# Kernel tuning notes

Measured on AMD Instinct MI355X. Metric: run time of the kernel, lower is better.

## Reference

```python
import jax, jax.numpy as jnp
import numpy as np

V, N, T, H, DK, DV, FF = 32000, 512, 43, 1024, 512, 512, 4096
EPS = 1e-5

def setup_inputs() -> dict:
    key = jax.random.key(0)
    ks = jax.random.split(key, 16)
    s = 0.02
    def p(k, shape):
        return jax.random.normal(k, shape, jnp.float32) * s
    return {
        "inputs": jax.random.randint(ks[0], (N, T), 0, V),
        "emb": p(ks[1], (V, H)),
        "pos": p(ks[2], (T, H)),
        "q1_w": p(ks[3], (H, DK)), "q1_b": jnp.zeros((DK,), jnp.float32),
        "k1_w": p(ks[4], (H, DK)), "k1_b": jnp.zeros((DK,), jnp.float32),
        "v1_w": p(ks[5], (H, DV)), "v1_b": jnp.zeros((DV,), jnp.float32),
        "q2_w": p(ks[6], (H, DK)), "q2_b": jnp.zeros((DK,), jnp.float32),
        "k2_w": p(ks[7], (H, DK)), "k2_b": jnp.zeros((DK,), jnp.float32),
        "v2_w": p(ks[8], (H, DV)), "v2_b": jnp.zeros((DV,), jnp.float32),
        "proj_w": p(ks[9], (2 * DV, H)), "proj_b": jnp.zeros((H,), jnp.float32),
        "ln_g": jnp.ones((H,), jnp.float32), "ln_b": jnp.zeros((H,), jnp.float32),
        "w1_w": p(ks[10], (H, FF)), "w1_b": jnp.zeros((FF,), jnp.float32),
        "w2_w": p(ks[11], (FF, H)), "w2_b": jnp.zeros((H,), jnp.float32),
        "fl_w": p(ks[12], (H, 1)), "fl_b": jnp.zeros((1,), jnp.float32),
    }

def reference(inputs, emb, pos, q1_w, q1_b, k1_w, k1_b, v1_w, v1_b,
              q2_w, q2_b, k2_w, k2_b, v2_w, v2_b, proj_w, proj_b,
              ln_g, ln_b, w1_w, w1_b, w2_w, w2_b, fl_w, fl_b):
    # embed: token + positional embeddings -> (N, T, H)
    x = emb[inputs] + pos[None, :, :]

    def ln(y):
        m = y.mean(-1, keepdims=True)
        v = ((y - m) ** 2).mean(-1, keepdims=True)  # unbiased=False, as torch LayerNorm
        return (y - m) / jnp.sqrt(v + EPS) * ln_g + ln_b

    def head(qw, qb, kw, kb, vw, vb):
        Q = x @ qw + qb            # (N,T,DK)
        K = x @ kw + kb            # (N,T,DK)
        Vh = x @ vw + vb           # (N,T,DV)
        scores = jnp.einsum('ntd,nsd->nts', Q, K) / jnp.sqrt(jnp.float32(DK))
        return jnp.einsum('nts,nsd->ntd', jax.nn.softmax(scores, axis=-1), Vh)

    attn = jnp.concatenate(
        [head(q1_w, q1_b, k1_w, k1_b, v1_w, v1_b),
         head(q2_w, q2_b, k2_w, k2_b, v2_w, v2_b)], axis=-1)  # (N,T,2*DV)
    h = ln(x + attn @ proj_w + proj_b)
    # FFN with ReLU (clamp(min=0)); NOTE: same LayerNorm params (norm_mh) reused
    h = ln(h + jnp.maximum(h @ w1_w + w1_b, 0.0) @ w2_w + w2_b)
    # final: sigmoid head on CLS (first) token -> (N,1)
    return jax.nn.sigmoid(h[:, 0, :] @ fl_w + fl_b)
```

## Files before the change

kernel.cpp:

```cpp
#include <hip/hip_runtime.h>
#include <math.h>

typedef float  f32x4  __attribute__((ext_vector_type(4)));
typedef short  bf16x8 __attribute__((ext_vector_type(8)));
typedef unsigned short u16;
typedef unsigned int   u32;
typedef unsigned short u16x2 __attribute__((ext_vector_type(2)));
typedef unsigned short u16x4 __attribute__((ext_vector_type(4)));
typedef unsigned short u16x8 __attribute__((ext_vector_type(8)));

constexpr int Tn = 43, Hd = 1024, Nb = 512;

__device__ __forceinline__ u16 f2bf(float f) {
    u32 u = __float_as_uint(f);
    u32 r = u + 0x7FFFu + ((u >> 16) & 1u);
    return (u16)(r >> 16);
}
__device__ __forceinline__ float bf2f(u16 h) {
    return __uint_as_float(((u32)h) << 16);
}
__device__ __forceinline__ void cvt8(const float* f, u16x8* hi, u16x8* lo) {
    #pragma unroll
    for (int j = 0; j < 8; ++j) {
        u16 h = f2bf(f[j]);
        (*hi)[j] = h;
        (*lo)[j] = f2bf(f[j] - bf2f(h));
    }
}
__device__ __forceinline__ void cvt8h(const float* f, u16x8* hi) {
    #pragma unroll
    for (int j = 0; j < 8; ++j) (*hi)[j] = f2bf(f[j]);
}

__device__ __forceinline__ void convT1_seg(const float* __restrict__ W,
                                           u16* __restrict__ Hi,
                                           int K, int N, int local, int t, char* lds)
{
    float (*tile)[33] = (float(*)[33])lds;
    const int tn = N >> 5;
    const int k0 = (local / tn) << 5, n0 = (local % tn) << 5;
    {
        int kk = t >> 3, nn = (t & 7) * 4;
        float4 v = *(const float4*)(W + (size_t)(k0 + kk) * N + n0 + nn);
        tile[kk][nn] = v.x; tile[kk][nn + 1] = v.y;
        tile[kk][nn + 2] = v.z; tile[kk][nn + 3] = v.w;
    }
    __syncthreads();
    {
        int nn = t >> 3, kk = (t & 7) * 4;
        u16x4 h;
        #pragma unroll
        for (int j = 0; j < 4; ++j) h[j] = f2bf(tile[kk + j][nn]);
        *(u16x4*)(Hi + (size_t)(n0 + nn) * K + k0 + kk) = h;
    }
}

__device__ __forceinline__ void convN1_seg(const float* __restrict__ src,
                                           u16* __restrict__ Hi, int local, int t)
{
    const size_t e = ((size_t)local * 256 + t) * 8;
    const float4* p = (const float4*)(src + e);
    float4 v0 = p[0], v1 = p[1];
    float f[8] = {v0.x, v0.y, v0.z, v0.w, v1.x, v1.y, v1.z, v1.w};
    u16x8 hv;
    cvt8h(f, &hv);
    *(u16x8*)(Hi + e) = hv;
}

__device__ __forceinline__ void gemm_dev(
    const u16* Ahi, const u16* Alo, int lda, size_t az,
    const u16* Bhi, int ldb, size_t bz,
    const float* bias, float* C, u16* CHi, u16* CLo, int ldc, int crz, int ccz,
    int M, int N, int K, int nz, int flags,
    float* Cp, size_t pstride, char* lds, int tid, int t0, int tstride)
{
    const bool RELU = flags & 1, PLANES = flags & 2, SPLIT = flags & 4;
    const bool A1 = flags & 8, PL1 = flags & 16;
    const int ncol = N >> 7;
    const int tpz = (M >> 6) * ncol;
    const int ntiles = nz * tpz;
    const int BOFF = A1 ? 8192 : 16384;

    const int ra = tid >> 2, ga = tid & 3;
    const int rb = tid >> 1, gb = (tid & 1) << 1;
    const int wA  = ((ra >> 4) << 10) | (ga << 8) | ((((ra & 15) ^ (ga << 1)) & 15) << 4);
    const int wB0 = ((rb >> 4) << 10) | (gb << 8) | ((((rb & 15) ^ (gb << 1)) & 15) << 4);
    const int wB1 = ((rb >> 4) << 10) | ((gb + 1) << 8) | ((((rb & 15) ^ ((gb + 1) << 1)) & 15) << 4);
    const int wv = tid >> 6, lane = tid & 63;
    const int wr = wv >> 1, wc = wv & 1;
    const int l15 = lane & 15, l4 = lane >> 4;
    const int rsw = (l15 ^ (l4 << 1)) << 4;
    int fA[2], fB[4];
    #pragma unroll
    for (int m = 0; m < 2; ++m) fA[m] = (((wr << 1) + m) << 10) | (l4 << 8) | rsw;
    #pragma unroll
    for (int n = 0; n < 4; ++n) fB[n] = (((wc << 2) + n) << 10) | (l4 << 8) | rsw;

    for (int t = t0; t < ntiles; t += tstride) {
        const int z = t / tpz, r = t - z * tpz;
        const int tm = r / ncol;
        const int bm = tm << 6, bn = (r - tm * ncol) << 7;
        int kc = K, kb = 0;
        const u16 *ah = Ahi, *al = Alo, *bh = Bhi;
        if (SPLIT) { kc = K / nz; kb = z * kc; }
        else { ah += z * az; if (!A1) al += z * az; bh += z * bz; }

        const u16* pAh = ah + (size_t)(bm + ra) * lda + kb + ga * 8;
        const u16* pAl = A1 ? pAh : al + (size_t)(bm + ra) * lda + kb + ga * 8;
        const u16* pBh = bh + (size_t)(bn + rb) * ldb + kb + gb * 8;

        f32x4 acc[2][4] = {};

        uint4 sAh0 = *(const uint4*)pAh,        sAh1 = *(const uint4*)(pAh + 32);
        uint4 sAl0, sAl1;
        if (!A1) { sAl0 = *(const uint4*)pAl;   sAl1 = *(const uint4*)(pAl + 32); }
        uint4 sB00 = *(const uint4*)pBh,        sB01 = *(const uint4*)(pBh + 8);
        uint4 sB10 = *(const uint4*)(pBh + 32), sB11 = *(const uint4*)(pBh + 40);

        for (int k0 = 0; k0 < kc; k0 += 64) {
            __syncthreads();
            *(uint4*)(lds + wA)        = sAh0;
            *(uint4*)(lds + 4096 + wA) = sAh1;
            if (!A1) {
                *(uint4*)(lds + 8192 + wA)  = sAl0;
                *(uint4*)(lds + 12288 + wA) = sAl1;
            }
            *(uint4*)(lds + BOFF + wB0)        = sB00;
            *(uint4*)(lds + BOFF + wB1)        = sB01;
            *(uint4*)(lds + BOFF + 8192 + wB0) = sB10;
            *(uint4*)(lds + BOFF + 8192 + wB1) = sB11;
            __syncthreads();
            if (k0 + 64 < kc) {
                pAh += 64; pBh += 64;
                sAh0 = *(const uint4*)pAh;        sAh1 = *(const uint4*)(pAh + 32);
                if (!A1) {
                    pAl += 64;
                    sAl0 = *(const uint4*)pAl;    sAl1 = *(const uint4*)(pAl + 32);
                }
                sB00 = *(const uint4*)pBh;        sB01 = *(const uint4*)(pBh + 8);
                sB10 = *(const uint4*)(pBh + 32); sB11 = *(const uint4*)(pBh + 40);
            }
            #pragma unroll
            for (int h = 0; h < 2; ++h) {
                bf16x8 a8[2], c8[2], b8[4];
                #pragma unroll
                for (int m = 0; m < 2; ++m) {
                    a8[m] = *(const bf16x8*)(lds + (h << 12) + fA[m]);
                    if (!A1) c8[m] = *(const bf16x8*)(lds + 8192 + (h << 12) + fA[m]);
                }
                #pragma unroll
                for (int n = 0; n < 4; ++n)
                    b8[n] = *(const bf16x8*)(lds + BOFF + (h << 13) + fB[n]);
                #pragma unroll
                for (int m = 0; m < 2; ++m)
                    #pragma unroll
                    for (int n = 0; n < 4; ++n) {
                        acc[m][n] = __builtin_amdgcn_mfma_f32_16x16x32_bf16(a8[m], b8[n], acc[m][n], 0, 0, 0);
                        if (!A1)
                            acc[m][n] = __builtin_amdgcn_mfma_f32_16x16x32_bf16(c8[m], b8[n], acc[m][n], 0, 0, 0);
                    }
            }
        }

        #pragma unroll
        for (int n = 0; n < 4; ++n) {
            const int col = bn + (wc << 6) + n * 16 + l15;
            const float bv = (!SPLIT && bias) ? bias[col] : 0.f;
            const int colz = SPLIT ? col : col + z * ccz;
            #pragma unroll
            for (int m = 0; m < 2; ++m) {
                const int row0 = bm + (wr << 5) + m * 16 + l4 * 4;
                #pragma unroll
                for (int rg = 0; rg < 4; ++rg) {
                    const int row = row0 + rg;
                    float v = acc[m][n][rg];
                    if (SPLIT) {
                        Cp[z * pstride + (size_t)row * N + col] = v;
                    } else {
                        const int rowz = row + z * crz;
                        v += bv;
                        if (RELU) v = fmaxf(v, 0.f);
                        if (PL1) {
                            CHi[(size_t)rowz * ldc + colz] = f2bf(v);
                        } else if (PLANES) {
                            u16 hh = f2bf(v);
                            CHi[(size_t)rowz * ldc + colz] = hh;
                            CLo[(size_t)rowz * ldc + colz] = f2bf(v - bf2f(hh));
                        } else {
                            C[(size_t)rowz * ldc + colz] = v;
                        }
                    }
                }
            }
        }
    }
}

__device__ __forceinline__ void gemm_G(
    const float* k1w, const float* k2w, const float* q1w, const float* q2w,
    u16* GHi, char* lds, int tid, int t0, int tstride)
{
    const int ra = tid >> 2, ga = tid & 3;
    const int rb = tid >> 1, gb = (tid & 1) << 1;
    const int wA  = ((ra >> 4) << 10) | (ga << 8) | ((((ra & 15) ^ (ga << 1)) & 15) << 4);
    const int wB0 = ((rb >> 4) << 10) | (gb << 8) | ((((rb & 15) ^ (gb << 1)) & 15) << 4);
    const int wB1 = ((rb >> 4) << 10) | ((gb + 1) << 8) | ((((rb & 15) ^ ((gb + 1) << 1)) & 15) << 4);
    const int wv = tid >> 6, lane = tid & 63;
    const int wr = wv >> 1, wc = wv & 1;
    const int l15 = lane & 15, l4 = lane >> 4;
    const int rsw = (l15 ^ (l4 << 1)) << 4;
    int fA[2], fB[4];
    #pragma unroll
    for (int m = 0; m < 2; ++m) fA[m] = (((wr << 1) + m) << 10) | (l4 << 8) | rsw;
    #pragma unroll
    for (int n = 0; n < 4; ++n) fB[n] = (((wc << 2) + n) << 10) | (l4 << 8) | rsw;

    for (int t = t0; t < 256; t += tstride) {
        const int z = t >> 7, r = t & 127;
        const int bm = (r >> 3) << 6, bn = (r & 7) << 7;
        const float* pA = (z ? k2w : k1w) + (size_t)(bm + ra) * 512 + ga * 8;
        const float* pB = (z ? q2w : q1w) + (size_t)(bn + rb) * 512 + gb * 8;

        f32x4 acc[2][4] = {};
        float4 a0 = ((const float4*)pA)[0], a1 = ((const float4*)pA)[1];
        float4 b0 = ((const float4*)pB)[0], b1 = ((const float4*)pB)[1];
        float4 b2 = ((const float4*)pB)[2], b3 = ((const float4*)pB)[3];

        for (int k0 = 0; k0 < 512; k0 += 32) {
            u16x8 hi, lo;
            float fa[8] = {a0.x, a0.y, a0.z, a0.w, a1.x, a1.y, a1.z, a1.w};
            float fb[8] = {b0.x, b0.y, b0.z, b0.w, b1.x, b1.y, b1.z, b1.w};
            float fc[8] = {b2.x, b2.y, b2.z, b2.w, b3.x, b3.y, b3.z, b3.w};
            __syncthreads();
            cvt8(fa, &hi, &lo);
            *(u16x8*)(lds + wA) = hi;
            *(u16x8*)(lds + 4096 + wA) = lo;
            cvt8h(fb, &hi);
            *(u16x8*)(lds + 8192 + wB0) = hi;
            cvt8h(fc, &hi);
            *(u16x8*)(lds + 8192 + wB1) = hi;
            __syncthreads();
            if (k0 + 32 < 512) {
                pA += 32; pB += 32;
                a0 = ((const float4*)pA)[0]; a1 = ((const float4*)pA)[1];
                b0 = ((const float4*)pB)[0]; b1 = ((const float4*)pB)[1];
                b2 = ((const float4*)pB)[2]; b3 = ((const float4*)pB)[3];
            }
            bf16x8 a8[2], c8[2], b8[4];
            #pragma unroll
            for (int m = 0; m < 2; ++m) {
                a8[m] = *(const bf16x8*)(lds + fA[m]);
                c8[m] = *(const bf16x8*)(lds + 4096 + fA[m]);
            }
            #pragma unroll
            for (int n = 0; n < 4; ++n)
                b8[n] = *(const bf16x8*)(lds + 8192 + fB[n]);
            #pragma unroll
            for (int m = 0; m < 2; ++m)
                #pragma unroll
                for (int n = 0; n < 4; ++n) {
                    acc[m][n] = __builtin_amdgcn_mfma_f32_16x16x32_bf16(a8[m], b8[n], acc[m][n], 0, 0, 0);
                    acc[m][n] = __builtin_amdgcn_mfma_f32_16x16x32_bf16(c8[m], b8[n], acc[m][n], 0, 0, 0);
                }
        }

        #pragma unroll
        for (int n = 0; n < 4; ++n) {
            const int col = bn + (wc << 6) + n * 16 + l15;
            #pragma unroll
            for (int m = 0; m < 2; ++m) {
                const int row0 = bm + (wr << 5) + m * 16 + l4 * 4;
                #pragma unroll
                for (int rg = 0; rg < 4; ++rg) {
                    const int row = z * 1024 + row0 + rg;
                    GHi[(size_t)row * 1024 + col] = f2bf(acc[m][n][rg]);
                }
            }
        }
    }
}

struct Args {
    const int* toks; const float* emb; const float* pos;
    const float *q1w, *q2w, *k1w, *k2w, *v1w, *v2w, *pw, *w1w, *w2w;
    const float *q1b, *q2b, *v1b, *v2b, *pb, *lg, *lb, *w1b, *w2b, *flw, *flb;
    u16 *GHi, *WpTHi, *W1THi, *W2THi, *WvNHi, *WvpHi;
    float *bU, *bvp;
    float* XclsF; u16 *XclsHi, *XclsLo;
    float* U; u16 *YHi, *YLo;
    float* Hb; u16 *HbHi, *HbLo;
    u16 *EHi, *ELo;
    float* Cp;
    float* out;
};

__global__ __launch_bounds__(256, 4)
void k1_kernel(Args A)
{
    __shared__ alignas(16) char lds[16384];
    const int id = blockIdx.x, t = threadIdx.x;
    const size_t HO = (size_t)1024 * 512;
    if (id < 256) {
        gemm_G(A.k1w, A.k2w, A.q1w, A.q2w, A.GHi, lds, t, id, 256);
    } else if (id < 768) {
        const int n = id - 256;
        const int tok = A.toks[n * Tn];
        float4 e = ((const float4*)(A.emb + (size_t)tok * Hd))[t];
        float4 p = ((const float4*)A.pos)[t];
        float f[4] = {e.x + p.x, e.y + p.y, e.z + p.z, e.w + p.w};
        ((float4*)(A.XclsF + (size_t)n * Hd))[t] = make_float4(f[0], f[1], f[2], f[3]);
        u16x4 hv, lv;
        #pragma unroll
        for (int j = 0; j < 4; ++j) {
            u16 h = f2bf(f[j]);
            hv[j] = h;
            lv[j] = f2bf(f[j] - bf2f(h));
        }
        *(u16x4*)(A.XclsHi + (size_t)n * Hd + t * 4) = hv;
        *(u16x4*)(A.XclsLo + (size_t)n * Hd + t * 4) = lv;
    } else if (id < 1280) {
        const int b = id - 768;
        const int wave = t >> 6, lane = t & 63;
        const int jj = b * 4 + wave;
        const int head = jj >> 10, j = jj & 1023;
        const float* row = (head ? A.k2w : A.k1w) + (size_t)j * 512;
        const float* bqp = head ? A.q2b : A.q1b;
        float4 r0 = ((const float4*)row)[lane * 2];
        float4 r1 = ((const float4*)row)[lane * 2 + 1];
        float4 b0 = ((const float4*)bqp)[lane * 2];
        float4 b1 = ((const float4*)bqp)[lane * 2 + 1];
        float d = r0.x*b0.x + r0.y*b0.y + r0.z*b0.z + r0.w*b0.w
                + r1.x*b1.x + r1.y*b1.y + r1.z*b1.z + r1.w*b1.w;
        #pragma unroll
        for (int off = 32; off; off >>= 1) d += __shfl_xor(d, off);
        if (lane == 0) A.bU[jj] = d;
    } else if (id < 2304) {
        convT1_seg(A.pw, A.WpTHi, 1024, 1024, id - 1280, t, lds);
    } else if (id < 2560) {
        convN1_seg(A.v1w, A.WvNHi, id - 2304, t);
    } else {
        convN1_seg(A.v2w, A.WvNHi + HO, id - 2560, t);
    }
}

__global__ __launch_bounds__(256, 4)
void k2_kernel(Args A)
{
    __shared__ alignas(16) char lds[32768];
    const int id = blockIdx.x, t = threadIdx.x;
    const size_t HO = (size_t)1024 * 512;
    if (id < 128)
        gemm_dev(A.XclsHi, A.XclsLo, 1024, 0, A.GHi, 1024, 0,
                 A.bU, A.U, nullptr, nullptr, 2048, 0, 0,
                 512, 2048, 1024, 1, 0, nullptr, 0, lds, t, id, 128);
    else if (id < 384)
        gemm_dev(A.WpTHi, nullptr, 1024, 512, A.WvNHi, 512, HO,
                 nullptr, nullptr, A.WvpHi, nullptr, 2048, 0, 1024,
                 1024, 1024, 512, 2, 8 | 16, nullptr, 0, lds, t, id - 128, 256);
    else if (id < 640) {
        const int wave = t >> 6, lane = t & 63;
        const int c = (id - 384) * 4 + wave;
        const int j0 = lane * 16;
        u16x8 h0 = *(const u16x8*)(A.WpTHi + (size_t)c * 1024 + j0);
        u16x8 h1 = *(const u16x8*)(A.WpTHi + (size_t)c * 1024 + j0 + 8);
        const float* bsrc = (j0 < 512) ? (A.v1b + j0) : (A.v2b + j0 - 512);
        float d = 0.f;
        #pragma unroll
        for (int j = 0; j < 8; ++j) d += bsrc[j] * bf2f(h0[j]);
        #pragma unroll
        for (int j = 0; j < 8; ++j) d += bsrc[8 + j] * bf2f(h1[j]);
        #pragma unroll
        for (int off = 32; off; off >>= 1) d += __shfl_xor(d, off);
        if (lane == 0) A.bvp[c] = d + A.pb[c];
    } else {
        convT1_seg(A.w1w, A.W1THi, 1024, 4096, id - 640, t, lds);
    }
}

__global__ __launch_bounds__(512, 1)
void k3_kernel(Args A)
{
    __shared__ float us[2048];
    __shared__ float ps[128];
    __shared__ u16 xc[Tn * 1024];
    const int n = blockIdx.x, tid = threadIdx.x;
    ((float4*)us)[tid] = ((const float4*)(A.U + (size_t)n * 2048))[tid];
    __syncthreads();

    const int wave = tid >> 6, lane = tid & 63;
    const int* tk = A.toks + n * Tn;
    for (int s = wave; s < Tn; s += 8) {
        const int tok = tk[s];
        const float4* er = (const float4*)(A.emb + (size_t)tok * Hd);
        const float4* pr = (const float4*)(A.pos + (size_t)s * Hd);
        float d1 = 0.f, d2 = 0.f;
        #pragma unroll
        for (int i = 0; i < 4; ++i) {
            const int c = i * 64 + lane;
            float4 e = er[c], p = pr[c];
            float x0 = e.x + p.x, x1 = e.y + p.y, x2 = e.z + p.z, x3 = e.w + p.w;
            u16x4 xv;
            xv[0] = f2bf(x0); xv[1] = f2bf(x1); xv[2] = f2bf(x2); xv[3] = f2bf(x3);
            *(u16x4*)(xc + s * 1024 + c * 4) = xv;
            const float* u1 = us + c * 4;
            const float* u2 = us + 1024 + c * 4;
            d1 += x0 * u1[0] + x1 * u1[1] + x2 * u1[2] + x3 * u1[3];
            d2 += x0 * u2[0] + x1 * u2[1] + x2 * u2[2] + x3 * u2[3];
        }
        #pragma unroll
        for (int off = 32; off; off >>= 1) {
            d1 += __shfl_xor(d1, off);
            d2 += __shfl_xor(d2, off);
        }
        if (lane == 0) {
            ps[s]      = d1 * 0.044194173824159216f;
            ps[64 + s] = d2 * 0.044194173824159216f;
        }
    }
    __syncthreads();
    if (wave < 2) {
        float v = (lane < Tn) ? ps[wave * 64 + lane] : -INFINITY;
        float mx = v;
        #pragma unroll
        for (int off = 32; off; off >>= 1) mx = fmaxf(mx, __shfl_xor(mx, off));
        float e = (lane < Tn) ? __expf(v - mx) : 0.f;
        float sum = e;
        #pragma unroll
        for (int off = 32; off; off >>= 1) sum += __shfl_xor(sum, off);
        if (lane < Tn) ps[wave * 64 + lane] = e / sum;
    }
    __syncthreads();

    float a1x = 0.f, a1y = 0.f, a2x = 0.f, a2y = 0.f;
    for (int s = 0; s < Tn; ++s) {
        const float p1 = ps[s], p2 = ps[64 + s];
        u16x2 xv = *(const u16x2*)(xc + s * 1024 + tid * 2);
        const float x0 = bf2f(xv[0]), x1 = bf2f(xv[1]);
        a1x = fmaf(p1, x0, a1x); a1y = fmaf(p1, x1, a1y);
        a2x = fmaf(p2, x0, a2x); a2y = fmaf(p2, x1, a2y);
    }
    u16x2 h1, l1, h2, l2;
    u16 h;
    h = f2bf(a1x); h1[0] = h; l1[0] = f2bf(a1x - bf2f(h));
    h = f2bf(a1y); h1[1] = h; l1[1] = f2bf(a1y - bf2f(h));
    h = f2bf(a2x); h2[0] = h; l2[0] = f2bf(a2x - bf2f(h));
    h = f2bf(a2y); h2[1] = h; l2[1] = f2bf(a2y - bf2f(h));
    const size_t o = (size_t)n * 2048 + tid * 2;
    *(u16x2*)(A.YHi + o) = h1;          *(u16x2*)(A.YLo + o) = l1;
    *(u16x2*)(A.YHi + o + 1024) = h2;   *(u16x2*)(A.YLo + o + 1024) = l2;
}

__global__ __launch_bounds__(256, 4)
void k4_kernel(Args A)
{
    __shared__ alignas(16) char lds[32768];
    const int id = blockIdx.x, t = threadIdx.x;
    if (id < 512)
        gemm_dev(A.YHi, A.YLo, 2048, 0, A.WvpHi, 2048, 0,
                 nullptr, nullptr, nullptr, nullptr, 0, 0, 0,
                 512, 1024, 2048, 8, 4, A.Cp, (size_t)Nb * Hd, lds, t, id, 512);
    else
        convT1_seg(A.w2w, A.W2THi, 4096, 1024, id - 512, t, lds);
}

__global__ __launch_bounds__(256)
void k5_kernel(Args A)
{
    const int tid = threadIdx.x;
    const size_t base = (size_t)blockIdx.x * Hd;
    const size_t P = (size_t)Nb * Hd;
    float4 v = ((const float4*)A.bvp)[tid];
    {
        float4 xc = ((const float4*)(A.XclsF + base))[tid];
        v.x += xc.x; v.y += xc.y; v.z += xc.z; v.w += xc.w;
    }
    #pragma unroll
    for (int z = 0; z < 8; ++z) {
        float4 c = ((const float4*)(A.Cp + z * P + base))[tid];
        v.x += c.x; v.y += c.y; v.z += c.z; v.w += c.w;
    }
    float s = v.x + v.y + v.z + v.w;
    float q = v.x*v.x + v.y*v.y + v.z*v.z + v.w*v.w;
    #pragma unroll
    for (int off = 32; off; off >>= 1) {
        s += __shfl_xor(s, off);
        q += __shfl_xor(q, off);
    }
    __shared__ float ss[4], sq[4];
    const int lane = tid & 63, w = tid >> 6;
    if (lane == 0) { ss[w] = s; sq[w] = q; }
    __syncthreads();
    s = ss[0] + ss[1] + ss[2] + ss[3];
    q = sq[0] + sq[1] + sq[2] + sq[3];
    const float mean = s * (1.f / Hd);
    const float var = q * (1.f / Hd) - mean * mean;
    const float rstd = rsqrtf(var + 1e-5f);
    float4 gv = ((const float4*)A.lg)[tid];
    float4 bv = ((const float4*)A.lb)[tid];
    float f[4];
    f[0] = (v.x - mean) * rstd * gv.x + bv.x;
    f[1] = (v.y - mean) * rstd * gv.y + bv.y;
    f[2] = (v.z - mean) * rstd * gv.z + bv.z;
    f[3] = (v.w - mean) * rstd * gv.w + bv.w;
    ((float4*)(A.Hb + base))[tid] = make_float4(f[0], f[1], f[2], f[3]);
    u16x4 hv, lv;
    #pragma unroll
    for (int j = 0; j < 4; ++j) {
        u16 hh = f2bf(f[j]);
        hv[j] = hh;
        lv[j] = f2bf(f[j] - bf2f(hh));
    }
    *(u16x4*)(A.HbHi + base + tid * 4) = hv;
    *(u16x4*)(A.HbLo + base + tid * 4) = lv;
}

__global__ __launch_bounds__(256, 4)
void k6_kernel(Args A)
{
    __shared__ alignas(16) char lds[32768];
    gemm_dev(A.HbHi, A.HbLo, 1024, 0, A.W1THi, 1024, 0,
             A.w1b, nullptr, A.EHi, A.ELo, 4096, 0, 0,
             512, 4096, 1024, 1, 3, nullptr, 0, lds, threadIdx.x, blockIdx.x, 256);
}

__global__ __launch_bounds__(256, 4)
void k7_kernel(Args A)
{
    __shared__ alignas(16) char lds[32768];
    gemm_dev(A.EHi, A.ELo, 4096, 0, A.W2THi, 4096, 0,
             nullptr, nullptr, nullptr, nullptr, 0, 0, 0,
             512, 1024, 4096, 4, 4, A.Cp, (size_t)Nb * Hd,
             lds, threadIdx.x, blockIdx.x, 256);
}

__global__ __launch_bounds__(256)
void k8_kernel(Args A)
{
    const int tid = threadIdx.x;
    const size_t base = (size_t)blockIdx.x * Hd;
    const size_t P = (size_t)Nb * Hd;
    float4 v = ((const float4*)A.w2b)[tid];
    {
        float4 hh = ((const float4*)(A.Hb + base))[tid];
        v.x += hh.x; v.y += hh.y; v.z += hh.z; v.w += hh.w;
    }
    #pragma unroll
    for (int z = 0; z < 4; ++z) {
        float4 c = ((const float4*)(A.Cp + z * P + base))[tid];
        v.x += c.x; v.y += c.y; v.z += c.z; v.w += c.w;
    }
    float s = v.x + v.y + v.z + v.w;
    float q = v.x*v.x + v.y*v.y + v.z*v.z + v.w*v.w;
    #pragma unroll
    for (int off = 32; off; off >>= 1) {
        s += __shfl_xor(s, off);
        q += __shfl_xor(q, off);
    }
    __shared__ float ss[4], sq[4], sd[4];
    const int lane = tid & 63, w = tid >> 6;
    if (lane == 0) { ss[w] = s; sq[w] = q; }
    __syncthreads();
    s = ss[0] + ss[1] + ss[2] + ss[3];
    q = sq[0] + sq[1] + sq[2] + sq[3];
    const float mean = s * (1.f / Hd);
    const float var = q * (1.f / Hd) - mean * mean;
    const float rstd = rsqrtf(var + 1e-5f);
    float4 gv = ((const float4*)A.lg)[tid];
    float4 bv = ((const float4*)A.lb)[tid];
    float4 wv = ((const float4*)A.flw)[tid];
    float d = ((v.x - mean) * rstd * gv.x + bv.x) * wv.x
            + ((v.y - mean) * rstd * gv.y + bv.y) * wv.y
            + ((v.z - mean) * rstd * gv.z + bv.z) * wv.z
            + ((v.w - mean) * rstd * gv.w + bv.w) * wv.w;
    #pragma unroll
    for (int off = 32; off; off >>= 1) d += __shfl_xor(d, off);
    if (lane == 0) sd[w] = d;
    __syncthreads();
    if (tid == 0) {
        float z = sd[0] + sd[1] + sd[2] + sd[3] + A.flb[0];
        A.out[blockIdx.x] = 1.f / (1.f + expf(-z));
    }
}

extern "C" void kernel_launch(void* const* d_in, const int* in_sizes, int n_in,
                              void* d_out, int out_size, void* d_ws, size_t ws_size,
                              hipStream_t stream)
{
    Args A;
    A.toks = (const int*)d_in[0];
    A.emb  = (const float*)d_in[1];
    A.pos  = (const float*)d_in[2];
    A.q1w = (const float*)d_in[3];  A.q1b = (const float*)d_in[4];
    A.k1w = (const float*)d_in[5];
    A.v1w = (const float*)d_in[7];  A.v1b = (const float*)d_in[8];
    A.q2w = (const float*)d_in[9];  A.q2b = (const float*)d_in[10];
    A.k2w = (const float*)d_in[11];
    A.v2w = (const float*)d_in[13]; A.v2b = (const float*)d_in[14];
    A.pw  = (const float*)d_in[15]; A.pb  = (const float*)d_in[16];
    A.lg  = (const float*)d_in[17]; A.lb  = (const float*)d_in[18];
    A.w1w = (const float*)d_in[19]; A.w1b = (const float*)d_in[20];
    A.w2w = (const float*)d_in[21]; A.w2b = (const float*)d_in[22];
    A.flw = (const float*)d_in[23]; A.flb = (const float*)d_in[24];
    A.out = (float*)d_out;
    char* wsb = (char*)d_ws;

    size_t off = 0;
    auto alloc = [&](size_t bytes) { size_t o = off; off = (off + bytes + 255) & ~(size_t)255; return o; };

    A.GHi   = (u16*)(wsb + alloc(2048 * 1024 * 2));
    A.WpTHi = (u16*)(wsb + alloc(1024 * 1024 * 2));
    A.W1THi = (u16*)(wsb + alloc(4096 * 1024 * 2));
    A.W2THi = (u16*)(wsb + alloc(1024 * 4096 * 2));
    A.WvNHi = (u16*)(wsb + alloc(2 * 1024 * 512 * 2));
    A.WvpHi = (u16*)(wsb + alloc(1024 * 2048 * 2));
    A.bU    = (float*)(wsb + alloc(2048 * 4));
    A.bvp   = (float*)(wsb + alloc(1024 * 4));
    A.XclsF = (float*)(wsb + alloc((size_t)Nb * Hd * 4));
    A.XclsHi= (u16*)(wsb + alloc((size_t)Nb * Hd * 2));
    A.XclsLo= (u16*)(wsb + alloc((size_t)Nb * Hd * 2));
    A.U     = (float*)(wsb + alloc((size_t)Nb * 2048 * 4));
    A.YHi   = (u16*)(wsb + alloc((size_t)Nb * 2048 * 2));
    A.YLo   = (u16*)(wsb + alloc((size_t)Nb * 2048 * 2));
    A.Hb    = (float*)(wsb + alloc((size_t)Nb * Hd * 4));
    A.HbHi  = (u16*)(wsb + alloc((size_t)Nb * Hd * 2));
    A.HbLo  = (u16*)(wsb + alloc((size_t)Nb * Hd * 2));
    A.EHi   = (u16*)(wsb + alloc((size_t)Nb * 4096 * 2));
    A.ELo   = (u16*)(wsb + alloc((size_t)Nb * 4096 * 2));
    A.Cp    = (float*)(wsb + alloc((size_t)8 * Nb * Hd * 4));

    k1_kernel<<<2816, 256, 0, stream>>>(A);
    k2_kernel<<<4736, 256, 0, stream>>>(A);
    k3_kernel<<<512,  512, 0, stream>>>(A);
    k4_kernel<<<4608, 256, 0, stream>>>(A);
    k5_kernel<<<512,  256, 0, stream>>>(A);
    k6_kernel<<<256,  256, 0, stream>>>(A);
    k7_kernel<<<256,  256, 0, stream>>>(A);
    k8_kernel<<<512,  256, 0, stream>>>(A);
}
```

Before: 114.4 us.

## Fuse residual+LayerNorm epilogues into split-K GEMMs via last-block atomic counters

Removes the separate k5 and k8 LayerNorm kernels. Each split-K GEMM block now increments a per-row-tile atomic counter, and the last block to finish a 64-row tile reduces the partials, applies LayerNorm and, in the final stage, the sigmoid head. This saves two kernel launches and their scheduling gaps. The cost is a serialized tail in which one block handles 64 rows on its own, plus a memset of the counters and reliance on the ordering that threadfence provides.

```diff
diff --git a/kernel.cpp b/kernel.cpp
--- a/kernel.cpp
+++ b/kernel.cpp
@@ -287,10 +287,12 @@
     u16 *GHi, *WpTHi, *W1THi, *W2THi, *WvNHi, *WvpHi;
     float *bU, *bvp;
     float* XclsF; u16 *XclsHi, *XclsLo;
-    float* U; u16 *YHi, *YLo;
+    u16 *YHi, *YLo;
+    float* U;
     float* Hb; u16 *HbHi, *HbLo;
     u16 *EHi, *ELo;
     float* Cp;
+    int *cnt1, *cnt2;
     float* out;
 };
 
@@ -455,63 +457,67 @@
 {
     __shared__ alignas(16) char lds[32768];
     const int id = blockIdx.x, t = threadIdx.x;
-    if (id < 512)
+    const size_t P = (size_t)Nb * Hd;
+    if (id < 512) {
         gemm_dev(A.YHi, A.YLo, 2048, 0, A.WvpHi, 2048, 0,
                  nullptr, nullptr, nullptr, nullptr, 0, 0, 0,
-                 512, 1024, 2048, 8, 4, A.Cp, (size_t)Nb * Hd, lds, t, id, 512);
-    else
+                 512, 1024, 2048, 8, 4, A.Cp, P, lds, t, id, 512);
+        const int tm = (id & 63) >> 3;
+        __threadfence();
+        int* flag = (int*)lds;
+        if (t == 0) *flag = atomicAdd(A.cnt1 + tm, 1);
+        __syncthreads();
+        if (*flag == 63) {
+            __threadfence();
+            float* shr = (float*)(lds + 64);
+            const int lane = t & 63, w = t >> 6;
+            for (int row = tm * 64; row < tm * 64 + 64; ++row) {
+                const size_t base = (size_t)row * Hd;
+                float4 v = ((const float4*)A.bvp)[t];
+                float4 xcv = ((const float4*)(A.XclsF + base))[t];
+                v.x += xcv.x; v.y += xcv.y; v.z += xcv.z; v.w += xcv.w;
+                #pragma unroll
+                for (int z = 0; z < 8; ++z) {
+                    float4 c = ((const float4*)(A.Cp + z * P + base))[t];
+                    v.x += c.x; v.y += c.y; v.z += c.z; v.w += c.w;
+                }
+                float s = v.x + v.y + v.z + v.w;
+                float q = v.x*v.x + v.y*v.y + v.z*v.z + v.w*v.w;
+                #pragma unroll
+                for (int off = 32; off; off >>= 1) {
+                    s += __shfl_xor(s, off);
+                    q += __shfl_xor(q, off);
+                }
+                if (lane == 0) { shr[w] = s; shr[4 + w] = q; }
+                __syncthreads();
+                s = shr[0] + shr[1] + shr[2] + shr[3];
+                q = shr[4] + shr[5] + shr[6] + shr[7];
+                __syncthreads();
+                const float mean = s * (1.f / Hd);
+                const float var = q * (1.f / Hd) - mean * mean;
+                const float rstd = rsqrtf(var + 1e-5f);
+                float4 gv = ((const float4*)A.lg)[t];
+                float4 bv = ((const float4*)A.lb)[t];
+                float f[4];
+                f[0] = (v.x - mean) * rstd * gv.x + bv.x;
+                f[1] = (v.y - mean) * rstd * gv.y + bv.y;
+                f[2] = (v.z - mean) * rstd * gv.z + bv.z;
+                f[3] = (v.w - mean) * rstd * gv.w + bv.w;
+                ((float4*)(A.Hb + base))[t] = make_float4(f[0], f[1], f[2], f[3]);
+                u16x4 hv, lv;
+                #pragma unroll
+                for (int j = 0; j < 4; ++j) {
+                    u16 hh = f2bf(f[j]);
+                    hv[j] = hh;
+                    lv[j] = f2bf(f[j] - bf2f(hh));
+                }
+                *(u16x4*)(A.HbHi + base + t * 4) = hv;
+                *(u16x4*)(A.HbLo + base + t * 4) = lv;
+            }
+        }
+    } else {
         convT1_seg(A.w2w, A.W2THi, 4096, 1024, id - 512, t, lds);
-}
-
-__global__ __launch_bounds__(256)
-void k5_kernel(Args A)
-{
-    const int tid = threadIdx.x;
-    const size_t base = (size_t)blockIdx.x * Hd;
-    const size_t P = (size_t)Nb * Hd;
-    float4 v = ((const float4*)A.bvp)[tid];
-    {
-        float4 xc = ((const float4*)(A.XclsF + base))[tid];
-        v.x += xc.x; v.y += xc.y; v.z += xc.z; v.w += xc.w;
-    }
-    #pragma unroll
-    for (int z = 0; z < 8; ++z) {
-        float4 c = ((const float4*)(A.Cp + z * P + base))[tid];
-        v.x += c.x; v.y += c.y; v.z += c.z; v.w += c.w;
-    }
-    float s = v.x + v.y + v.z + v.w;
-    float q = v.x*v.x + v.y*v.y + v.z*v.z + v.w*v.w;
-    #pragma unroll
-    for (int off = 32; off; off >>= 1) {
-        s += __shfl_xor(s, off);
-        q += __shfl_xor(q, off);
-    }
-    __shared__ float ss[4], sq[4];
-    const int lane = tid & 63, w = tid >> 6;
-    if (lane == 0) { ss[w] = s; sq[w] = q; }
-    __syncthreads();
-    s = ss[0] + ss[1] + ss[2] + ss[3];
-    q = sq[0] + sq[1] + sq[2] + sq[3];
-    const float mean = s * (1.f / Hd);
-    const float var = q * (1.f / Hd) - mean * mean;
-    const float rstd = rsqrtf(var + 1e-5f);
-    float4 gv = ((const float4*)A.lg)[tid];
-    float4 bv = ((const float4*)A.lb)[tid];
-    float f[4];
-    f[0] = (v.x - mean) * rstd * gv.x + bv.x;
-    f[1] = (v.y - mean) * rstd * gv.y + bv.y;
-    f[2] = (v.z - mean) * rstd * gv.z + bv.z;
-    f[3] = (v.w - mean) * rstd * gv.w + bv.w;
-    ((float4*)(A.Hb + base))[tid] = make_float4(f[0], f[1], f[2], f[3]);
-    u16x4 hv, lv;
-    #pragma unroll
-    for (int j = 0; j < 4; ++j) {
-        u16 hh = f2bf(f[j]);
-        hv[j] = hh;
-        lv[j] = f2bf(f[j] - bf2f(hh));
-    }
-    *(u16x4*)(A.HbHi + base + tid * 4) = hv;
-    *(u16x4*)(A.HbLo + base + tid * 4) = lv;
+    }
 }
 
 __global__ __launch_bounds__(256, 4)
@@ -527,58 +533,62 @@
 void k7_kernel(Args A)
 {
     __shared__ alignas(16) char lds[32768];
+    const int id = blockIdx.x, t = threadIdx.x;
+    const size_t P = (size_t)Nb * Hd;
     gemm_dev(A.EHi, A.ELo, 4096, 0, A.W2THi, 4096, 0,
              nullptr, nullptr, nullptr, nullptr, 0, 0, 0,
-             512, 1024, 4096, 4, 4, A.Cp, (size_t)Nb * Hd,
-             lds, threadIdx.x, blockIdx.x, 256);
-}
-
-__global__ __launch_bounds__(256)
-void k8_kernel(Args A)
-{
-    const int tid = threadIdx.x;
-    const size_t base = (size_t)blockIdx.x * Hd;
-    const size_t P = (size_t)Nb * Hd;
-    float4 v = ((const float4*)A.w2b)[tid];
-    {
-        float4 hh = ((const float4*)(A.Hb + base))[tid];
-        v.x += hh.x; v.y += hh.y; v.z += hh.z; v.w += hh.w;
-    }
-    #pragma unroll
-    for (int z = 0; z < 4; ++z) {
-        float4 c = ((const float4*)(A.Cp + z * P + base))[tid];
-        v.x += c.x; v.y += c.y; v.z += c.z; v.w += c.w;
-    }
-    float s = v.x + v.y + v.z + v.w;
-    float q = v.x*v.x + v.y*v.y + v.z*v.z + v.w*v.w;
-    #pragma unroll
-    for (int off = 32; off; off >>= 1) {
-        s += __shfl_xor(s, off);
-        q += __shfl_xor(q, off);
-    }
-    __shared__ float ss[4], sq[4], sd[4];
-    const int lane = tid & 63, w = tid >> 6;
-    if (lane == 0) { ss[w] = s; sq[w] = q; }
+             512, 1024, 4096, 4, 4, A.Cp, P, lds, t, id, 256);
+    const int tm = (id & 63) >> 3;
+    __threadfence();
+    int* flag = (int*)lds;
+    if (t == 0) *flag = atomicAdd(A.cnt2 + tm, 1);
     __syncthreads();
-    s = ss[0] + ss[1] + ss[2] + ss[3];
-    q = sq[0] + sq[1] + sq[2] + sq[3];
-    const float mean = s * (1.f / Hd);
-    const float var = q * (1.f / Hd) - mean * mean;
-    const float rstd = rsqrtf(var + 1e-5f);
-    float4 gv = ((const float4*)A.lg)[tid];
-    float4 bv = ((const float4*)A.lb)[tid];
-    float4 wv = ((const float4*)A.flw)[tid];
-    float d = ((v.x - mean) * rstd * gv.x + bv.x) * wv.x
-            + ((v.y - mean) * rstd * gv.y + bv.y) * wv.y
-            + ((v.z - mean) * rstd * gv.z + bv.z) * wv.z
-            + ((v.w - mean) * rstd * gv.w + bv.w) * wv.w;
-    #pragma unroll
-    for (int off = 32; off; off >>= 1) d += __shfl_xor(d, off);
-    if (lane == 0) sd[w] = d;
-    __syncthreads();
-    if (tid == 0) {
-        float z = sd[0] + sd[1] + sd[2] + sd[3] + A.flb[0];
-        A.out[blockIdx.x] = 1.f / (1.f + expf(-z));
+    if (*flag == 31) {
+        __threadfence();
+        float* shr = (float*)(lds + 64);
+        const int lane = t & 63, w = t >> 6;
+        for (int row = tm * 64; row < tm * 64 + 64; ++row) {
+            const size_t base = (size_t)row * Hd;
+            float4 v = ((const float4*)A.w2b)[t];
+            float4 hh4 = ((const float4*)(A.Hb + base))[t];
+            v.x += hh4.x; v.y += hh4.y; v.z += hh4.z; v.w += hh4.w;
+            #pragma unroll
+            for (int z = 0; z < 4; ++z) {
+                float4 c = ((const float4*)(A.Cp + z * P + base))[t];
+                v.x += c.x; v.y += c.y; v.z += c.z; v.w += c.w;
+            }
+            float s = v.x + v.y + v.z + v.w;
+            float q = v.x*v.x + v.y*v.y + v.z*v.z + v.w*v.w;
+            #pragma unroll
+            for (int off = 32; off; off >>= 1) {
+                s += __shfl_xor(s, off);
+                q += __shfl_xor(q, off);
+            }
+            if (lane == 0) { shr[w] = s; shr[4 + w] = q; }
+            __syncthreads();
+            s = shr[0] + shr[1] + shr[2] + shr[3];
+            q = shr[4] + shr[5] + shr[6] + shr[7];
+            __syncthreads();
+            const float mean = s * (1.f / Hd);
+            const float var = q * (1.f / Hd) - mean * mean;
+            const float rstd = rsqrtf(var + 1e-5f);
+            float4 gv = ((const float4*)A.lg)[t];
+            float4 bv = ((const float4*)A.lb)[t];
+            float4 wv = ((const float4*)A.flw)[t];
+            float d = ((v.x - mean) * rstd * gv.x + bv.x) * wv.x
+                    + ((v.y - mean) * rstd * gv.y + bv.y) * wv.y
+                    + ((v.z - mean) * rstd * gv.z + bv.z) * wv.z
+                    + ((v.w - mean) * rstd * gv.w + bv.w) * wv.w;
+            #pragma unroll
+            for (int off = 32; off; off >>= 1) d += __shfl_xor(d, off);
+            if (lane == 0) shr[8 + w] = d;
+            __syncthreads();
+            if (t == 0) {
+                float z2 = shr[8] + shr[9] + shr[10] + shr[11] + A.flb[0];
+                A.out[row] = 1.f / (1.f + expf(-z2));
+            }
+            __syncthreads();
+        }
     }
 }
 
@@ -627,13 +637,15 @@
     A.EHi   = (u16*)(wsb + alloc((size_t)Nb * 4096 * 2));
     A.ELo   = (u16*)(wsb + alloc((size_t)Nb * 4096 * 2));
     A.Cp    = (float*)(wsb + alloc((size_t)8 * Nb * Hd * 4));
+    A.cnt1  = (int*)(wsb + alloc(64 * 4));
+    A.cnt2  = (int*)(wsb + alloc(64 * 4));
+
+    hipMemsetAsync(A.cnt1, 0, 128 * 4, stream);
 
     k1_kernel<<<2816, 256, 0, stream>>>(A);
     k2_kernel<<<4736, 256, 0, stream>>>(A);
     k3_kernel<<<512,  512, 0, stream>>>(A);
     k4_kernel<<<4608, 256, 0, stream>>>(A);
-    k5_kernel<<<512,  256, 0, stream>>>(A);
     k6_kernel<<<256,  256, 0, stream>>>(A);
     k7_kernel<<<256,  256, 0, stream>>>(A);
-    k8_kernel<<<512,  256, 0, stream>>>(A);
-}
+}
```

Measured after the change: 390.8 us. 242% more time.
